# Kernel tuning notes

Hardware: AMD Instinct MI355X
Metric: run time of the kernel (lower is better)

Reference implementation:

```python
import jax, jax.numpy as jnp
import numpy as np

BERT = 178  # BERT_VECTOR_SIZE
WLEN = 20   # letters per word (dim1 = WLEN + BERT)


def _lstm(x, h0, c0, Wih, Whh, bih, bhh):
    """PyTorch-convention LSTM (gate order i,f,g,o). x: [B,T,D] -> outputs [B,T,H]."""
    xg = jnp.einsum('btd,gd->btg', x, Wih) + bih + bhh  # precompute input projections

    def step(carry, xt):
        h, c = carry
        g = xt + h @ Whh.T
        i, f, gg, o = jnp.split(g, 4, axis=-1)
        c = jax.nn.sigmoid(f) * c + jax.nn.sigmoid(i) * jnp.tanh(gg)
        h = jax.nn.sigmoid(o) * jnp.tanh(c)
        return (h, c), h

    _, hs = jax.lax.scan(step, (h0, c0), jnp.swapaxes(xg, 0, 1))
    return jnp.swapaxes(hs, 0, 1)  # [B,T,H]


def setup_inputs() -> dict:
    key = jax.random.key(0)
    ks = jax.random.split(key, 32)
    B, S, L = 32, 64, 50          # batch, sentence_length, number_of_letters
    Hs, Hm, D, O = 128, 256, 128, 32  # secondary_hidden, main_hidden, word_dims, output_size
    NW = B * S
    T = WLEN + BERT
    Din = D + BERT                # sentence LSTM input size = 306
    s = 0.05
    rn = lambda k, sh: jax.random.normal(k, sh, dtype=jnp.float32)
    return {
        'X': rn(ks[0], (B, S, T, L)),
        'h0w': rn(ks[1], (NW, Hs)), 'c0w': rn(ks[2], (NW, Hs)),
        'h0f': rn(ks[3], (B, Hm)), 'c0f': rn(ks[4], (B, Hm)),
        'h0b': rn(ks[5], (B, Hm)), 'c0b': rn(ks[6], (B, Hm)),
        'Wih_w': rn(ks[7], (4 * Hs, L)) * s, 'Whh_w': rn(ks[8], (4 * Hs, Hs)) * s,
        'bih_w': rn(ks[9], (4 * Hs,)) * s, 'bhh_w': rn(ks[10], (4 * Hs,)) * s,
        'Wl': rn(ks[11], (D, Hs)) * s, 'bl': rn(ks[12], (D,)) * s,
        'Wih_f': rn(ks[13], (4 * Hm, Din)) * s, 'Whh_f': rn(ks[14], (4 * Hm, Hm)) * s,
        'bih_f': rn(ks[15], (4 * Hm,)) * s, 'bhh_f': rn(ks[16], (4 * Hm,)) * s,
        'Wih_b': rn(ks[17], (4 * Hm, Din)) * s, 'Whh_b': rn(ks[18], (4 * Hm, Hm)) * s,
        'bih_b': rn(ks[19], (4 * Hm,)) * s, 'bhh_b': rn(ks[20], (4 * Hm,)) * s,
        'Wo': rn(ks[21], (O, 2 * Hm)) * s, 'bo': rn(ks[22], (O,)) * s,
    }


def reference(X, h0w, c0w, h0f, c0f, h0b, c0b,
              Wih_w, Whh_w, bih_w, bhh_w, Wl, bl,
              Wih_f, Whh_f, bih_f, bhh_f,
              Wih_b, Whh_b, bih_b, bhh_b, Wo, bo):
    B, S = X.shape[0], X.shape[1]
    L = X.shape[-1]
    NW = B * S
    Xw = X.reshape(NW, -1, L)            # [NW, WLEN+BERT, L]
    letters = Xw[:, :WLEN, :]            # [NW, WLEN, L]
    bert = Xw[:, -BERT:, 0]              # vectorized replacement of the double loop

    out_w = _lstm(letters, h0w, c0w, Wih_w, Whh_w, bih_w, bhh_w)
    word_rep = out_w[:, -1, :] @ Wl.T + bl        # [NW, D]
    word_rep = jnp.concatenate([word_rep, bert], axis=1)  # [NW, D+BERT]
    sentences = word_rep.reshape(B, S, -1)

    out_f = _lstm(sentences, h0f, c0f, Wih_f, Whh_f, bih_f, bhh_f)
    out_b = _lstm(sentences[:, ::-1, :], h0b, c0b, Wih_b, Whh_b, bih_b, bhh_b)[:, ::-1, :]
    out = jnp.concatenate([out_f, out_b], axis=-1)  # [B, S, 2*Hm]

    words = out.reshape(NW, -1)
    tags = words @ Wo.T + bo
    return jax.nn.softmax(tags, axis=1)
```

## Files before the change

kernel.cpp:

```cpp
#include <hip/hip_runtime.h>
#include <cstdint>
#include <cstddef>

#define DI static __device__ __forceinline__

using half_t  = _Float16;
using half2_t = __attribute__((ext_vector_type(2))) _Float16;
using half8_t = __attribute__((ext_vector_type(8))) _Float16;
using f32x4_t = __attribute__((ext_vector_type(4))) float;

DI uint32_t pack2(float a, float b){ half2_t h; h[0]=(half_t)a; h[1]=(half_t)b; return __builtin_bit_cast(uint32_t,h); }
DI uint16_t f16b(float a){ return __builtin_bit_cast(uint16_t,(half_t)a); }
DI float lo16(uint32_t u){ half2_t h=__builtin_bit_cast(half2_t,u); return (float)h[0]; }
DI float hi16(uint32_t u){ half2_t h=__builtin_bit_cast(half2_t,u); return (float)h[1]; }
DI float fdot2(uint32_t w, uint32_t x, float acc){
  return __builtin_amdgcn_fdot2(__builtin_bit_cast(half2_t,w), __builtin_bit_cast(half2_t,x), acc, false);
}
DI float sigm(float x){ return __builtin_amdgcn_rcpf(1.f + __expf(-x)); }
DI float tanhf_(float x){ return 1.f - 2.f*__builtin_amdgcn_rcpf(__expf(2.f*x)+1.f); }

#define SROW 308
#define HSTR 280

#define N0 32768
#define N1 16384
#define N2 8192
#define N3 512
#define N4 262144
#define N5 313344
#define N6 2048
#define N7 8192
#define N8 364544
#define NTOT (N0+N1+N2+N3+N4+N5+N6+N7+N8)

__global__ void k_prep(const float* __restrict__ X,
                       const float* __restrict__ Wih_w, const float* __restrict__ Whh_w,
                       const float* __restrict__ bih_w, const float* __restrict__ bhh_w,
                       const float* __restrict__ Wl,
                       const float* __restrict__ Wih_f, const float* __restrict__ Whh_f,
                       const float* __restrict__ bih_f, const float* __restrict__ bhh_f,
                       const float* __restrict__ Wih_b, const float* __restrict__ Whh_b,
                       const float* __restrict__ bih_b, const float* __restrict__ bhh_b,
                       const float* __restrict__ Wo,
                       uint32_t* __restrict__ wWsw, uint32_t* __restrict__ wWxw,
                       uint32_t* __restrict__ wWlf, float* __restrict__ wbsw,
                       uint32_t* __restrict__ wWs, uint32_t* __restrict__ wWihs,
                       float* __restrict__ wbss, uint32_t* __restrict__ wWo,
                       float* __restrict__ sent)
{
  for (int i = blockIdx.x*blockDim.x + threadIdx.x; i < NTOT; i += gridDim.x*blockDim.x) {
    int id = i;
    if (id < N0) {
      int kp = id & 63, ng = id >> 6;
      int w = ng>>6, g = (ng>>4)&3, jl = ng&15;
      const float* s = Whh_w + (size_t)(g*128 + w*16 + jl)*128 + 2*kp;
      wWsw[id] = pack2(s[0], s[1]);
    } else if ((id -= N0) < N1) {
      int kp = id & 31, ng = id >> 5;
      int w = ng>>6, g = (ng>>4)&3, jl = ng&15;
      if (kp < 25) {
        const float* s = Wih_w + (size_t)(g*128 + w*16 + jl)*50 + 2*kp;
        wWxw[id] = pack2(s[0], s[1]);
      } else wWxw[id] = 0u;
    } else if ((id -= N1) < N2) {
      int kp = id & 63, d = id >> 6;
      const float* s = Wl + (size_t)d*128 + 2*kp;
      wWlf[id] = pack2(s[0], s[1]);
    } else if ((id -= N2) < N3) {
      int g = id & 3, j = id>>2;
      wbsw[id] = bih_w[g*128+j] + bhh_w[g*128+j];
    } else if ((id -= N3) < N4) {
      int kp = id & 127, ng = (id>>7)&1023, dir = id>>17;
      int w = ng>>7, g = (ng>>5)&3, jl = ng&31;
      int row = g*256 + w*32 + jl;
      const float* s = (dir ? Whh_b : Whh_f) + (size_t)row*256 + 2*kp;
      wWs[id] = pack2(s[0], s[1]);
    } else if ((id -= N4) < N5) {
      int dir = id >= 156672; int r = id - dir*156672;
      int g = r & 3, j = (r>>2)&255, kp = r>>10;
      const float* s = (dir ? Wih_b : Wih_f) + (size_t)(g*256+j)*306 + 2*kp;
      wWihs[id] = pack2(s[0], s[1]);
    } else if ((id -= N5) < N6) {
      int g = id & 3, j = (id>>2)&255, dir = id>>10;
      int row = g*256+j;
      wbss[id] = dir ? (bih_b[row]+bhh_b[row]) : (bih_f[row]+bhh_f[row]);
    } else if ((id -= N6) < N7) {
      int o = id & 31, kp = id>>5;
      const float* s = Wo + (size_t)o*512 + 2*kp;
      wWo[id] = pack2(s[0], s[1]);
    } else { id -= N7;
      int wg = id / 178, ii = id % 178;
      sent[(size_t)wg*SROW + 128 + ii] = X[(size_t)wg*9900 + (20+ii)*50];
    }
  }
}

__global__ __launch_bounds__(512, 2) void k_word(
    const float* __restrict__ X, const float* __restrict__ h0w, const float* __restrict__ c0w,
    const uint32_t* __restrict__ wWsw, const uint32_t* __restrict__ wWxw,
    const float* __restrict__ wbsw, const uint32_t* __restrict__ wWlf,
    const float* __restrict__ bl, float* __restrict__ sent)
{
  __shared__ __align__(16) uint32_t lets[11520];
  __shared__ __align__(16) uint16_t hbuf[2][2176];
  const int tid = threadIdx.x;
  const int wave = tid >> 6, lane = tid & 63;
  const int l15 = lane & 15, l4 = lane >> 4;
  const int wg0 = blockIdx.x * 16;

  uint4 Bh[4][4], Bx[4][2];
  #pragma unroll
  for (int g = 0; g < 4; ++g) {
    int ng = wave*64 + g*16 + l15;
    #pragma unroll
    for (int Kt = 0; Kt < 4; ++Kt) Bh[g][Kt] = *(const uint4*)(wWsw + ng*64 + Kt*16 + l4*4);
    #pragma unroll
    for (int Kt = 0; Kt < 2; ++Kt) Bx[g][Kt] = *(const uint4*)(wWxw + ng*32 + Kt*16 + l4*4);
  }
  for (int i = tid; i < 11520; i += 512) {
    int c = i % 36, mt = i / 36; int m = mt & 15, t = mt >> 4;
    lets[i] = (c < 25) ? pack2(X[(size_t)(wg0+m)*9900 + t*50 + 2*c],
                               X[(size_t)(wg0+m)*9900 + t*50 + 2*c + 1]) : 0u;
  }
  for (int i = tid; i < 2048; i += 512) {
    int m = i >> 7, k = i & 127;
    hbuf[0][m*136 + k] = f16b(h0w[(size_t)(wg0+m)*128 + k]);
  }
  const float4 bs = *(const float4*)(wbsw + (wave*16 + l15)*4);
  float cr[4];
  #pragma unroll
  for (int r = 0; r < 4; ++r) cr[r] = c0w[(size_t)(wg0 + l4*4 + r)*128 + wave*16 + l15];
  __syncthreads();

  uint16_t* hc = hbuf[0];
  uint16_t* hn = hbuf[1];
  const uint16_t* lp = (const uint16_t*)lets;
  #pragma unroll 1
  for (int t = 0; t < 20; ++t) {
    f32x4_t acc[4];
    acc[0] = (f32x4_t){bs.x,bs.x,bs.x,bs.x};
    acc[1] = (f32x4_t){bs.y,bs.y,bs.y,bs.y};
    acc[2] = (f32x4_t){bs.z,bs.z,bs.z,bs.z};
    acc[3] = (f32x4_t){bs.w,bs.w,bs.w,bs.w};
    #pragma unroll
    for (int Kt = 0; Kt < 2; ++Kt) {
      uint4 av = *(const uint4*)(lp + (t*16 + l15)*72 + Kt*32 + l4*8);
      half8_t a = __builtin_bit_cast(half8_t, av);
      #pragma unroll
      for (int g = 0; g < 4; ++g)
        acc[g] = __builtin_amdgcn_mfma_f32_16x16x32_f16(a, __builtin_bit_cast(half8_t, Bx[g][Kt]), acc[g], 0,0,0);
    }
    #pragma unroll
    for (int Kt = 0; Kt < 4; ++Kt) {
      uint4 av = *(const uint4*)(hc + l15*136 + Kt*32 + l4*8);
      half8_t a = __builtin_bit_cast(half8_t, av);
      #pragma unroll
      for (int g = 0; g < 4; ++g)
        acc[g] = __builtin_amdgcn_mfma_f32_16x16x32_f16(a, __builtin_bit_cast(half8_t, Bh[g][Kt]), acc[g], 0,0,0);
    }
    #pragma unroll
    for (int r = 0; r < 4; ++r) {
      float cc = sigm(acc[1][r])*cr[r] + sigm(acc[0][r])*tanhf_(acc[2][r]);
      cr[r] = cc;
      float hh = sigm(acc[3][r])*tanhf_(cc);
      hn[(l4*4+r)*136 + wave*16 + l15] = f16b(hh);
    }
    uint16_t* tp = hc; hc = hn; hn = tp;
    __syncthreads();
  }
  uint4 Bl[4];
  #pragma unroll
  for (int Kt = 0; Kt < 4; ++Kt) Bl[Kt] = *(const uint4*)(wWlf + (wave*16 + l15)*64 + Kt*16 + l4*4);
  f32x4_t a2 = (f32x4_t){0.f,0.f,0.f,0.f};
  #pragma unroll
  for (int Kt = 0; Kt < 4; ++Kt) {
    uint4 av = *(const uint4*)(hc + l15*136 + Kt*32 + l4*8);
    a2 = __builtin_amdgcn_mfma_f32_16x16x32_f16(__builtin_bit_cast(half8_t, av),
                                                __builtin_bit_cast(half8_t, Bl[Kt]), a2, 0,0,0);
  }
  const float blv = bl[wave*16 + l15];
  #pragma unroll
  for (int r = 0; r < 4; ++r)
    sent[(size_t)(wg0 + l4*4 + r)*SROW + wave*16 + l15] = a2[r] + blv;
}

__global__ __launch_bounds__(256) void k_sxg(
    const float* __restrict__ sent, const uint32_t* __restrict__ Wihs,
    const float* __restrict__ bss, uint2* __restrict__ xgq)
{
  __shared__ uint32_t x16[153*8];
  const int tid = threadIdx.x;
  const int dir = blockIdx.x >> 8, rg = blockIdx.x & 255;
  for (int i = tid; i < 153*8; i += 256) {
    int r = i & 7, kp = i >> 3;
    int ot = rg*8 + r; int b = ot >> 6, tt = ot & 63;
    int si = dir ? (63 - tt) : tt;
    const float* s = sent + (size_t)(b*64 + si)*SROW + 2*kp;
    x16[kp*8 + r] = pack2(s[0], s[1]);
  }
  __syncthreads();
  const int j = tid;
  float acc[8][4];
  {
    const float4 b4 = *(const float4*)(bss + (dir*256 + j)*4);
    #pragma unroll
    for (int r = 0; r < 8; ++r) { acc[r][0]=b4.x; acc[r][1]=b4.y; acc[r][2]=b4.z; acc[r][3]=b4.w; }
  }
  for (int kp = 0; kp < 153; ++kp) {
    uint4 wv = *(const uint4*)(Wihs + ((size_t)(dir*153 + kp)*256 + j)*4);
    uint4 xa = *(const uint4*)(x16 + kp*8);
    uint4 xb = *(const uint4*)(x16 + kp*8 + 4);
    uint32_t wa[4] = {wv.x,wv.y,wv.z,wv.w};
    uint32_t xs[8] = {xa.x,xa.y,xa.z,xa.w,xb.x,xb.y,xb.z,xb.w};
    #pragma unroll
    for (int r = 0; r < 8; ++r)
      #pragma unroll
      for (int g = 0; g < 4; ++g) acc[r][g] = fdot2(wa[g], xs[r], acc[r][g]);
  }
  const int w = j >> 5, jh2 = (j >> 4) & 1, l15j = j & 15;
  #pragma unroll
  for (int r = 0; r < 8; ++r) {
    int ot = rg*8 + r; int b = ot >> 6, tt = ot & 63;
    int half = b >> 4, l4m = (b >> 2) & 3, rm = b & 3;
    uint2 v; v.x = pack2(acc[r][0], acc[r][1]); v.y = pack2(acc[r][2], acc[r][3]);
    size_t idx = ((((size_t)(dir*64 + tt)*2 + half)*8 + w)*2 + jh2)*256 + l15j*16 + l4m*4 + rm;
    xgq[idx] = v;
  }
}

__global__ __launch_bounds__(512, 2) void k_srec(
    const uint32_t* __restrict__ Ws, const float* __restrict__ h0f, const float* __restrict__ c0f,
    const float* __restrict__ h0b, const float* __restrict__ c0b,
    const uint2* __restrict__ xgq, uint16_t* __restrict__ outfb)
{
  extern __shared__ char smem[];
  uint16_t* h16a = (uint16_t*)(smem + 131072);
  uint16_t* h16b = h16a + 16*HSTR;
  const int tid = threadIdx.x;
  const int wave = tid >> 6, lane = tid & 63;
  const int dir = blockIdx.x >> 1, half = blockIdx.x & 1, m0 = half * 16;
  const int l15 = lane & 15, l4 = lane >> 4;

  uint4 Breg[8][6];
  #pragma unroll
  for (int Nt = 0; Nt < 8; ++Nt) {
    #pragma unroll
    for (int Kt = 0; Kt < 8; ++Kt) {
      int ng = wave*128 + Nt*16 + l15;
      uint4 v = *(const uint4*)(Ws + (size_t)(dir*1024 + ng)*128 + Kt*16 + l4*4);
      if (Kt < 6) Breg[Nt][Kt] = v;
      else *(uint4*)(smem + (((wave*16 + Nt*2 + (Kt-6))*64 + lane)*16)) = v;
    }
  }
  {
    const float* h0 = dir ? h0b : h0f;
    for (int i = tid; i < 16*256; i += 512) {
      int m = i >> 8, k = i & 255;
      h16a[m*HSTR + k] = f16b(h0[(size_t)(m0+m)*256 + k]);
    }
  }
  float cr[2][4];
  {
    const float* c0 = dir ? c0b : c0f;
    #pragma unroll
    for (int jh = 0; jh < 2; ++jh)
      #pragma unroll
      for (int r = 0; r < 4; ++r)
        cr[jh][r] = c0[(size_t)(m0 + l4*4 + r)*256 + wave*32 + jh*16 + l15];
  }
  __syncthreads();

  const char* xbase = (const char*)xgq + (size_t)dir*4194304 + half*32768;
  const uint32_t xlane = wave*4096 + l15*128 + l4*32;
  const int s0 = dir ? 63 : 0;
  const int sdelta = dir ? -65536 : 65536;
  const char* obase = (const char*)outfb + (size_t)s0*65536 + half*32768 + dir*16384;
  const uint32_t olane = (l4*4)*512 + wave*64 + l15*2;
  const uint32_t aoff = l15*HSTR + l4*8;

  uint16_t* hc = h16a;
  uint16_t* hn = h16b;

  uint4 p0 = *(const uint4*)(xbase + xlane);
  uint4 p1 = *(const uint4*)(xbase + xlane + 16);
  uint4 p2 = *(const uint4*)(xbase + xlane + 2048);
  uint4 p3 = *(const uint4*)(xbase + xlane + 2064);

  #pragma unroll 1
  for (int t = 0; t < 64; ++t) {
    f32x4_t acc[8];
    acc[0] = (f32x4_t){lo16(p0.x), lo16(p0.z), lo16(p1.x), lo16(p1.z)};
    acc[2] = (f32x4_t){hi16(p0.x), hi16(p0.z), hi16(p1.x), hi16(p1.z)};
    acc[4] = (f32x4_t){lo16(p0.y), lo16(p0.w), lo16(p1.y), lo16(p1.w)};
    acc[6] = (f32x4_t){hi16(p0.y), hi16(p0.w), hi16(p1.y), hi16(p1.w)};
    acc[1] = (f32x4_t){lo16(p2.x), lo16(p2.z), lo16(p3.x), lo16(p3.z)};
    acc[3] = (f32x4_t){hi16(p2.x), hi16(p2.z), hi16(p3.x), hi16(p3.z)};
    acc[5] = (f32x4_t){lo16(p2.y), lo16(p2.w), lo16(p3.y), lo16(p3.w)};
    acc[7] = (f32x4_t){hi16(p2.y), hi16(p2.w), hi16(p3.y), hi16(p3.w)};

    #pragma unroll
    for (int Kt = 0; Kt < 8; ++Kt) {
      uint4 av = *(const uint4*)(hc + aoff + Kt*32);
      half8_t a = __builtin_bit_cast(half8_t, av);
      #pragma unroll
      for (int Nt = 0; Nt < 8; ++Nt) {
        uint4 bv;
        if (Kt < 6) bv = Breg[Nt][Kt];
        else bv = *(const uint4*)(smem + (((wave*16 + Nt*2 + (Kt-6))*64 + lane)*16));
        acc[Nt] = __builtin_amdgcn_mfma_f32_16x16x32_f16(a, __builtin_bit_cast(half8_t, bv), acc[Nt], 0,0,0);
      }
    }

    p0 = *(const uint4*)(xbase + xlane + 65536);
    p1 = *(const uint4*)(xbase + xlane + 65536 + 16);
    p2 = *(const uint4*)(xbase + xlane + 65536 + 2048);
    p3 = *(const uint4*)(xbase + xlane + 65536 + 2064);

    #pragma unroll
    for (int jh = 0; jh < 2; ++jh) {
      #pragma unroll
      for (int r = 0; r < 4; ++r) {
        float gi = acc[0+jh][r], gf = acc[2+jh][r], gg = acc[4+jh][r], go = acc[6+jh][r];
        float ef = __expf(-gf), ei = __expf(-gi), eg = __expf(-2.f*gg);
        float pef = 1.f + ef, pei = 1.f + ei, peg = 1.f + eg;
        float num = cr[jh][r]*pei*peg + (1.f - eg)*pef;
        float cc  = num * __builtin_amdgcn_rcpf(pef*pei*peg);
        cr[jh][r] = cc;
        float ec = __expf(-2.f*cc), eo = __expf(-go);
        float hh = (1.f - ec) * __builtin_amdgcn_rcpf((1.f + ec)*(1.f + eo));
        uint16_t hb = f16b(hh);
        hn[(l4*4+r)*HSTR + wave*32 + jh*16 + l15] = hb;
        *(uint16_t*)(obase + olane + r*512 + jh*32) = hb;
      }
    }
    { uint16_t* tp = hc; hc = hn; hn = tp; }
    xbase += 65536;
    obase += sdelta;
    asm volatile("s_waitcnt lgkmcnt(0)\ns_barrier" ::: "memory");
  }
}

__global__ __launch_bounds__(256) void k_tags(
    const uint16_t* __restrict__ outfb, const uint32_t* __restrict__ Wo16,
    const float* __restrict__ bo, float* __restrict__ out)
{
  __shared__ uint32_t xr[8*256];
  const int tid = threadIdx.x;
  const int w0 = blockIdx.x * 8;
  const uint32_t* src = (const uint32_t*)outfb;
  for (int i = tid; i < 2048; i += 256) {
    int w = i >> 8, kp = i & 255;
    int widx = w0 + w;
    int s = widx & 63, q = widx >> 6;
    int half = q >> 4, m = q & 15;
    int dir = kp >> 7, wv = (kp >> 4) & 7, jh = (kp >> 3) & 1, l15h = kp & 7;
    xr[i] = src[s*16384 + half*8192 + dir*4096 + m*128 + wv*16 + jh*8 + l15h];
  }
  __syncthreads();
  const int o = tid & 31, w = tid >> 5;
  float a = bo[o];
  for (int kp = 0; kp < 256; ++kp)
    a = fdot2(Wo16[kp*32 + o], xr[w*256 + kp], a);
  float mx = a;
  #pragma unroll
  for (int off = 16; off; off >>= 1) mx = fmaxf(mx, __shfl_xor(mx, off, 32));
  float e = __expf(a - mx);
  float ssum = e;
  #pragma unroll
  for (int off = 16; off; off >>= 1) ssum += __shfl_xor(ssum, off, 32);
  out[(size_t)(w0+w)*32 + o] = e * __builtin_amdgcn_rcpf(ssum);
}

extern "C" void kernel_launch(void* const* d_in, const int* in_sizes, int n_in,
                              void* d_out, int out_size, void* d_ws, size_t ws_size,
                              hipStream_t stream) {
  const float* X     = (const float*)d_in[0];
  const float* h0w   = (const float*)d_in[1];
  const float* c0w   = (const float*)d_in[2];
  const float* h0f   = (const float*)d_in[3];
  const float* c0f   = (const float*)d_in[4];
  const float* h0b   = (const float*)d_in[5];
  const float* c0b   = (const float*)d_in[6];
  const float* Wih_w = (const float*)d_in[7];
  const float* Whh_w = (const float*)d_in[8];
  const float* bih_w = (const float*)d_in[9];
  const float* bhh_w = (const float*)d_in[10];
  const float* Wl    = (const float*)d_in[11];
  const float* bl    = (const float*)d_in[12];
  const float* Wih_f = (const float*)d_in[13];
  const float* Whh_f = (const float*)d_in[14];
  const float* bih_f = (const float*)d_in[15];
  const float* bhh_f = (const float*)d_in[16];
  const float* Wih_b = (const float*)d_in[17];
  const float* Whh_b = (const float*)d_in[18];
  const float* bih_b = (const float*)d_in[19];
  const float* bhh_b = (const float*)d_in[20];
  const float* Wo    = (const float*)d_in[21];
  const float* bo    = (const float*)d_in[22];

  char* ws = (char*)d_ws;
  uint32_t* wWsw  = (uint32_t*)(ws + 0);
  uint32_t* wWxw  = (uint32_t*)(ws + 131072);
  uint32_t* wWlf  = (uint32_t*)(ws + 196608);
  float*    wbsw  = (float*)   (ws + 229376);
  uint32_t* wWs   = (uint32_t*)(ws + 231424);
  uint32_t* wWihs = (uint32_t*)(ws + 1280000);
  float*    wbss  = (float*)   (ws + 2533376);
  uint32_t* wWo   = (uint32_t*)(ws + 2541568);
  float*    sent  = (float*)   (ws + 2574336);
  uint2*    xgq   = (uint2*)   (ws + 5097472);
  uint16_t* outfb = (uint16_t*)(ws + 13486080);

  hipFuncSetAttribute((const void*)k_srec, hipFuncAttributeMaxDynamicSharedMemorySize, 148992);

  k_prep<<<2048, 256, 0, stream>>>(X, Wih_w, Whh_w, bih_w, bhh_w, Wl, Wih_f, Whh_f, bih_f, bhh_f,
                                   Wih_b, Whh_b, bih_b, bhh_b, Wo,
                                   wWsw, wWxw, wWlf, wbsw, wWs, wWihs, wbss, wWo, sent);
  k_word<<<128, 512, 0, stream>>>(X, h0w, c0w, wWsw, wWxw, wbsw, wWlf, bl, sent);
  k_sxg<<<512, 256, 0, stream>>>(sent, wWihs, wbss, xgq);
  k_srec<<<4, 512, 148992, stream>>>(wWs, h0f, c0f, h0b, c0b, xgq, outfb);
  k_tags<<<256, 256, 0, stream>>>(outfb, wWo, bo, (float*)d_out);
}
```

Measured before the change: 310.7 us.

## Overlap LSTM gate math for even tiles with MFMAs of odd tiles

```diff
diff --git a/kernel.cpp b/kernel.cpp
--- a/kernel.cpp
+++ b/kernel.cpp
@@ -281,6 +281,20 @@
   uint16_t* hc = h16a;
   uint16_t* hn = h16b;
 
+#define UPD1(JH, R, GI, GF, GG, GO) {                                         \
+    float eo = __expf(-(GO));                         \
+    float ef = __expf(-(GF)), ei = __expf(-(GI)), eg = __expf(-2.f*(GG));     \
+    float pef = 1.f + ef, pei = 1.f + ei, peg = 1.f + eg;                     \
+    float num = cr[JH][R]*pei*peg + (1.f - eg)*pef;                           \
+    float cc  = num * __builtin_amdgcn_rcpf(pef*pei*peg);                     \
+    cr[JH][R] = cc;                                                           \
+    float ec = __expf(-2.f*cc);                                               \
+    float hh = (1.f - ec) * __builtin_amdgcn_rcpf((1.f + ec)*(1.f + eo));     \
+    uint16_t hb = f16b(hh);                                                   \
+    hn[(l4*4+(R))*HSTR + wave*32 + (JH)*16 + l15] = hb;                       \
+    *(uint16_t*)(obase + olane + (R)*512 + (JH)*32) = hb;                     \
+  }
+
   uint4 p0 = *(const uint4*)(xbase + xlane);
   uint4 p1 = *(const uint4*)(xbase + xlane + 16);
   uint4 p2 = *(const uint4*)(xbase + xlane + 2048);
@@ -298,18 +312,41 @@
     acc[5] = (f32x4_t){lo16(p2.y), lo16(p2.w), lo16(p3.y), lo16(p3.w)};
     acc[7] = (f32x4_t){hi16(p2.y), hi16(p2.w), hi16(p3.y), hi16(p3.w)};
 
+    __builtin_amdgcn_s_setprio(1);
     #pragma unroll
     for (int Kt = 0; Kt < 8; ++Kt) {
       uint4 av = *(const uint4*)(hc + aoff + Kt*32);
       half8_t a = __builtin_bit_cast(half8_t, av);
       #pragma unroll
-      for (int Nt = 0; Nt < 8; ++Nt) {
+      for (int g = 0; g < 4; ++g) {
+        const int Nt = g*2;
         uint4 bv;
         if (Kt < 6) bv = Breg[Nt][Kt];
         else bv = *(const uint4*)(smem + (((wave*16 + Nt*2 + (Kt-6))*64 + lane)*16));
         acc[Nt] = __builtin_amdgcn_mfma_f32_16x16x32_f16(a, __builtin_bit_cast(half8_t, bv), acc[Nt], 0,0,0);
       }
     }
+    __builtin_amdgcn_s_setprio(0);
+
+    #pragma unroll
+    for (int Kt = 0; Kt < 8; ++Kt) {
+      uint4 av = *(const uint4*)(hc + aoff + Kt*32);
+      half8_t a = __builtin_bit_cast(half8_t, av);
+      #pragma unroll
+      for (int g = 0; g < 4; ++g) {
+        const int Nt = g*2 + 1;
+        uint4 bv;
+        if (Kt < 6) bv = Breg[Nt][Kt];
+        else bv = *(const uint4*)(smem + (((wave*16 + Nt*2 + (Kt-6))*64 + lane)*16));
+        acc[Nt] = __builtin_amdgcn_mfma_f32_16x16x32_f16(a, __builtin_bit_cast(half8_t, bv), acc[Nt], 0,0,0);
+      }
+      if (Kt & 1) {
+        const int r = Kt >> 1;
+        UPD1(0, r, acc[0][r], acc[2][r], acc[4][r], acc[6][r]);
+        __builtin_amdgcn_sched_group_barrier(0x008, 8, 0);
+        __builtin_amdgcn_sched_group_barrier(0x002, 44, 0);
+      }
+    }
 
     p0 = *(const uint4*)(xbase + xlane + 65536);
     p1 = *(const uint4*)(xbase + xlane + 65536 + 16);
@@ -317,27 +354,15 @@
     p3 = *(const uint4*)(xbase + xlane + 65536 + 2064);
 
     #pragma unroll
-    for (int jh = 0; jh < 2; ++jh) {
-      #pragma unroll
-      for (int r = 0; r < 4; ++r) {
-        float gi = acc[0+jh][r], gf = acc[2+jh][r], gg = acc[4+jh][r], go = acc[6+jh][r];
-        float ef = __expf(-gf), ei = __expf(-gi), eg = __expf(-2.f*gg);
-        float pef = 1.f + ef, pei = 1.f + ei, peg = 1.f + eg;
-        float num = cr[jh][r]*pei*peg + (1.f - eg)*pef;
-        float cc  = num * __builtin_amdgcn_rcpf(pef*pei*peg);
-        cr[jh][r] = cc;
-        float ec = __expf(-2.f*cc), eo = __expf(-go);
-        float hh = (1.f - ec) * __builtin_amdgcn_rcpf((1.f + ec)*(1.f + eo));
-        uint16_t hb = f16b(hh);
-        hn[(l4*4+r)*HSTR + wave*32 + jh*16 + l15] = hb;
-        *(uint16_t*)(obase + olane + r*512 + jh*32) = hb;
-      }
-    }
+    for (int r = 0; r < 4; ++r)
+      UPD1(1, r, acc[1][r], acc[3][r], acc[5][r], acc[7][r]);
+
     { uint16_t* tp = hc; hc = hn; hn = tp; }
     xbase += 65536;
     obase += sdelta;
     asm volatile("s_waitcnt lgkmcnt(0)\ns_barrier" ::: "memory");
   }
+#undef UPD1
 }
 
 __global__ __launch_bounds__(256) void k_tags(
```

After: 306.3 us. About the same (-1.4%).
